# Kernel optimization log

Hardware: AMD Instinct MI355X
Metric: run time of the kernel (lower is better)

The kernel has to match this reference:

```python
import jax, jax.numpy as jnp
import numpy as np

N = 1024      # number of atoms
L = 64        # latent_size
VOCAB = 20    # vocab_size (len(ATOM_CATEGORIES))


def _lin(key, fan_in, fan_out):
    # mimic torch nn.Linear init: U(-1/sqrt(fan_in), 1/sqrt(fan_in))
    kw, kb = jax.random.split(key)
    s = 1.0 / np.sqrt(fan_in)
    W = jax.random.uniform(kw, (fan_in, fan_out), minval=-s, maxval=s, dtype=jnp.float32)
    b = jax.random.uniform(kb, (fan_out,), minval=-s, maxval=s, dtype=jnp.float32)
    return W, b


def setup_inputs() -> dict:
    key = jax.random.key(0)
    ks = jax.random.split(key, 9)
    We1, be1 = _lin(ks[3], 2 * L + 1, L)   # mlp_e layer 1
    We2, be2 = _lin(ks[4], L, L)           # mlp_e layer 2
    Wh1, bh1 = _lin(ks[5], L + 1, L)       # mlp_h layer 1
    Wh2, bh2 = _lin(ks[6], L, L)           # mlp_h layer 2
    Wo, bo = _lin(ks[7], L, 1)             # output_mlp
    return {
        "atom_categories": jax.random.randint(ks[0], (N,), 0, VOCAB),
        "atom_coordinates": jax.random.normal(ks[1], (N, 3), dtype=jnp.float32),
        "learnable_matrix": jax.random.normal(ks[2], (VOCAB, L), dtype=jnp.float32),
        "We1": We1, "be1": be1, "We2": We2, "be2": be2,
        "Wh1": Wh1, "bh1": bh1, "Wh2": Wh2, "bh2": bh2,
        "Wo": Wo, "bo": bo,
    }


def reference(atom_categories, atom_coordinates, learnable_matrix,
              We1, be1, We2, be2, Wh1, bh1, Wh2, bh2, Wo, bo):
    Z = atom_coordinates
    # init_H: learnable_matrix.T @ one_hot(cat) == row gather
    H = learnable_matrix[atom_categories]                       # [N, L]

    # pairwise squared distances ||Z_i - Z_j||^2
    d2 = jnp.sum((Z[:, None, :] - Z[None, :, :]) ** 2, axis=-1)  # [N, N]

    # mlp_e layer 1 on concat(H_i, H_j, d2): split We1 to avoid materializing concat
    W1i, W1j, w1z = We1[:L], We1[L:2 * L], We1[2 * L]            # [L,L],[L,L],[L]
    pre_i = H @ W1i                                              # [N, L]
    pre_j = H @ W1j                                              # [N, L]
    h1 = jnp.tanh(pre_i[:, None, :] + pre_j[None, :, :]
                  + d2[:, :, None] * w1z + be1)                  # [N, N, L]
    W_e = jnp.tanh(h1 @ We2 + be2)                               # [N, N, L]

    # V[i] = sum over j != i of sum_l W_e[i,j,l]
    total = jnp.sum(W_e, axis=(1, 2))                            # [N]
    diag = jnp.einsum('iil->i', W_e)                             # [N]
    V = total - diag                                             # [N]

    # mlp_h on concat(H_i, V_i): split Wh1
    hh = jnp.tanh(H @ Wh1[:L] + V[:, None] * Wh1[L] + bh1)       # [N, L]
    newH = jnp.tanh(hh @ Wh2 + bh2)                              # [N, L]

    Hsum = jnp.sum(newH, axis=0)                                 # [L]
    return (Hsum @ Wo + bo)[0]                                   # scalar
```

## Files before the change

### kernel.cpp

```cpp
#include <hip/hip_runtime.h>
#include <hip/hip_bf16.h>


#define N_ATOMS 1024
#define L_DIM 64
#define TPB 512
#define CSCALE 2.8853900817779268f

typedef _Float16 f16x8 __attribute__((ext_vector_type(8)));
typedef __fp16  fp16x2 __attribute__((ext_vector_type(2)));
typedef float f32x4 __attribute__((ext_vector_type(4)));

__device__ __forceinline__ float tanh_fast(float x) {
    float e = __builtin_amdgcn_exp2f(x * CSCALE);
    float r = __builtin_amdgcn_rcpf(e + 1.0f);
    return fmaf(-2.0f, r, 1.0f);
}

__global__ __launch_bounds__(256) void k_prep(const int* __restrict__ cat,
                                              const float* __restrict__ LM,
                                              const float* __restrict__ We1,
                                              const float* __restrict__ be1,
                                              float* __restrict__ H,
                                              float* __restrict__ preI,
                                              float* __restrict__ P3,
                                              float* __restrict__ out) {
    int t = threadIdx.x;
    int sub = t >> 6, l = t & 63;
    int i = blockIdx.x * 4 + sub;
    if (blockIdx.x == 0 && t == 0) out[0] = 0.f;
    __shared__ float hrow[4][L_DIM];
    float hv = LM[cat[i] * L_DIM + l];
    hrow[sub][l] = hv;
    H[i * L_DIM + l] = hv;
    __syncthreads();
    float s1 = 0.f, s2 = 0.f;
#pragma unroll
    for (int m = 0; m < L_DIM; m++) {
        float h = hrow[sub][m];
        s1 = fmaf(h, We1[m * L_DIM + l], s1);
        s2 = fmaf(h, We1[(L_DIM + m) * L_DIM + l], s2);
    }
    preI[i * L_DIM + l] = s1 * CSCALE;
    int cc = i >> 4;
    int Ll = i & 15;
    int quad = (l >> 3) & 3;
    int L = quad * 16 + Ll;
    int g = ((l >> 5) << 1) | ((l >> 2) & 1);
    int e2 = l & 3;
    P3[cc * 1024 + g * 256 + L * 4 + e2] = (s2 + be1[l]) * CSCALE;
}

__global__ __launch_bounds__(TPB) void k_main(const float* __restrict__ Z,
                                              const float* __restrict__ We1,
                                              const float* __restrict__ We2,
                                              const float* __restrict__ be2,
                                              const float* __restrict__ preI,
                                              const float* __restrict__ P3,
                                              const float* __restrict__ H,
                                              const float* __restrict__ Wh1,
                                              const float* __restrict__ bh1,
                                              const float* __restrict__ Wh2,
                                              const float* __restrict__ bh2,
                                              const float* __restrict__ Wo,
                                              const float* __restrict__ bo,
                                              float* __restrict__ out) {
    int i = blockIdx.x;
    int t = threadIdx.x;
    int lane = t & 63;
    int wave = t >> 6;
    int nlo = lane & 15;
    int quad = lane >> 4;

    __shared__ float d2s[N_ATOMS];
    __shared__ float red[TPB];
    __shared__ float hrow_s[L_DIM];
    __shared__ float hh_s[L_DIM];
    __shared__ float dgt[L_DIM];
    __shared__ f16x8 bLs[8 * 64];

    float zi0 = Z[i * 3], zi1 = Z[i * 3 + 1], zi2 = Z[i * 3 + 2];
    for (int p = t; p < N_ATOMS; p += TPB) {
        float a = zi0 - Z[p * 3], b = zi1 - Z[p * 3 + 1], c = zi2 - Z[p * 3 + 2];
        d2s[p] = a * a + b * b + c * c;
    }

    f32x4 aiR[4], wzR[4];
#pragma unroll
    for (int g = 0; g < 4; g++) {
        int mb = ((g >> 1) << 5) + (quad << 3) + ((g & 1) << 2);
        aiR[g] = *(const f32x4*)(preI + i * L_DIM + mb);
        f32x4 wz = *(const f32x4*)(We1 + 2 * L_DIM * L_DIM + mb);
        wzR[g] = wz * CSCALE;
    }

    f16x8 bH[4][2];
    float biasR[4];
#pragma unroll
    for (int nt = 0; nt < 4; nt++) {
        float psum = 0.f;
#pragma unroll
        for (int kt = 0; kt < 2; kt++) {
            f16x8 hi8, lo8;
#pragma unroll
            for (int e = 0; e < 8; e++) {
                float x = We2[(kt * 32 + quad * 8 + e) * L_DIM + nt * 16 + nlo];
                psum += x;
                float wp = -2.0f * CSCALE * x;
                _Float16 hi = (_Float16)wp;
                hi8[e] = hi;
                lo8[e] = (_Float16)(wp - (float)hi);
            }
            bH[nt][kt] = hi8;
            if (wave == 0) bLs[(kt * 4 + nt) * 64 + lane] = lo8;
        }
        psum += __shfl_xor(psum, 16);
        psum += __shfl_xor(psum, 32);
        biasR[nt] = CSCALE * (be2[nt * 16 + nlo] + psum);
    }

    const float* Pbase = P3 + (wave * 8) * 1024 + lane * 4;
    f32x4 p0 = *(const f32x4*)(Pbase + 0 * 256) + aiR[0];
    f32x4 p1 = *(const f32x4*)(Pbase + 1 * 256) + aiR[1];
    f32x4 p2 = *(const f32x4*)(Pbase + 2 * 256) + aiR[2];
    f32x4 p3 = *(const f32x4*)(Pbase + 3 * 256) + aiR[3];

    __syncthreads();

    f32x4 Vr4 = {0.f, 0.f, 0.f, 0.f};
    for (int k = 0; k < 8; k++) {
        int j0 = (wave * 8 + k) * 16;
        float d2 = d2s[j0 + nlo];
        f32x4 d2v = {d2, d2, d2, d2};

        f32x4 z0 = p0 + d2v * wzR[0];
        f32x4 z1 = p1 + d2v * wzR[1];
        f32x4 z2 = p2 + d2v * wzR[2];
        f32x4 z3 = p3 + d2v * wzR[3];
        f32x4 ex0, ex1, ex2, ex3;
#pragma unroll
        for (int e = 0; e < 4; e++) {
            ex0[e] = __builtin_amdgcn_exp2f(z0[e]);
            ex1[e] = __builtin_amdgcn_exp2f(z1[e]);
            ex2[e] = __builtin_amdgcn_exp2f(z2[e]);
            ex3[e] = __builtin_amdgcn_exp2f(z3[e]);
        }
        ex0 += 1.0f; ex1 += 1.0f; ex2 += 1.0f; ex3 += 1.0f;
        f32x4 r0, r1, r2, r3;
#pragma unroll
        for (int e = 0; e < 4; e++) {
            r0[e] = __builtin_amdgcn_rcpf(ex0[e]);
            r1[e] = __builtin_amdgcn_rcpf(ex1[e]);
            r2[e] = __builtin_amdgcn_rcpf(ex2[e]);
            r3[e] = __builtin_amdgcn_rcpf(ex3[e]);
        }
        union { f16x8 v; fp16x2 h2[4]; } u0, u1;
        u0.h2[0] = __builtin_amdgcn_cvt_pkrtz(r0[0], r0[1]);
        u0.h2[1] = __builtin_amdgcn_cvt_pkrtz(r0[2], r0[3]);
        u0.h2[2] = __builtin_amdgcn_cvt_pkrtz(r1[0], r1[1]);
        u0.h2[3] = __builtin_amdgcn_cvt_pkrtz(r1[2], r1[3]);
        u1.h2[0] = __builtin_amdgcn_cvt_pkrtz(r2[0], r2[1]);
        u1.h2[1] = __builtin_amdgcn_cvt_pkrtz(r2[2], r2[3]);
        u1.h2[2] = __builtin_amdgcn_cvt_pkrtz(r3[0], r3[1]);
        u1.h2[3] = __builtin_amdgcn_cvt_pkrtz(r3[2], r3[3]);
        f16x8 aH0 = u0.v, aH1 = u1.v;

        if (k < 7) {
            const float* nb = Pbase + (k + 1) * 1024;
            p0 = *(const f32x4*)(nb + 0 * 256) + aiR[0];
            p1 = *(const f32x4*)(nb + 1 * 256) + aiR[1];
            p2 = *(const f32x4*)(nb + 2 * 256) + aiR[2];
            p3 = *(const f32x4*)(nb + 3 * 256) + aiR[3];
        }

#pragma unroll
        for (int nt = 0; nt < 4; nt++) {
            f16x8 bl0 = bLs[(0 * 4 + nt) * 64 + lane];
            f16x8 bl1 = bLs[(1 * 4 + nt) * 64 + lane];
            f32x4 acc = {biasR[nt], biasR[nt], biasR[nt], biasR[nt]};
            acc = __builtin_amdgcn_mfma_f32_16x16x32_f16(aH0, bH[nt][0], acc, 0, 0, 0);
            acc = __builtin_amdgcn_mfma_f32_16x16x32_f16(aH0, bl0, acc, 0, 0, 0);
            acc = __builtin_amdgcn_mfma_f32_16x16x32_f16(aH1, bH[nt][1], acc, 0, 0, 0);
            acc = __builtin_amdgcn_mfma_f32_16x16x32_f16(aH1, bl1, acc, 0, 0, 0);
            f32x4 ev;
#pragma unroll
            for (int r4 = 0; r4 < 4; r4++) ev[r4] = __builtin_amdgcn_exp2f(acc[r4]);
            ev += 1.0f;
            f32x4 rv;
#pragma unroll
            for (int r4 = 0; r4 < 4; r4++) rv[r4] = __builtin_amdgcn_rcpf(ev[r4]);
            Vr4 += rv;
        }
    }

    red[t] = Vr4[0] + Vr4[1] + Vr4[2] + Vr4[3];
    __syncthreads();

    float Rall;
    if (t < 64) {
        float r = red[t];
#pragma unroll
        for (int w = 1; w < 8; w++) r += red[t + 64 * w];
#pragma unroll
        for (int o = 32; o > 0; o >>= 1) r += __shfl_xor(r, o);
        Rall = r;
        int cc = i >> 4, Ll = i & 15;
        int q2 = (t >> 3) & 3;
        int g = ((t >> 5) << 1) | ((t >> 2) & 1);
        float z = preI[i * L_DIM + t] + P3[cc * 1024 + g * 256 + (q2 * 16 + Ll) * 4 + (t & 3)];
        float rr = __builtin_amdgcn_rcpf(__builtin_amdgcn_exp2f(z) + 1.0f);
        dgt[t] = fmaf(-2.0f, rr, 1.0f);
        hrow_s[t] = H[i * L_DIM + t];
    }
    __syncthreads();
    if (t < 64) {
        float S = be2[t];
#pragma unroll
        for (int m = 0; m < L_DIM; m++) S = fmaf(dgt[m], We2[m * L_DIM + t], S);
        float rd = __builtin_amdgcn_rcpf(__builtin_amdgcn_exp2f(S * CSCALE) + 1.0f);
#pragma unroll
        for (int o = 32; o > 0; o >>= 1) rd += __shfl_xor(rd, o);
        float V = fmaf(-2.0f, Rall - rd, (float)(1023 * L_DIM));
        float s = 0.f;
#pragma unroll
        for (int m = 0; m < L_DIM; m++) s = fmaf(hrow_s[m], Wh1[m * L_DIM + t], s);
        s = fmaf(V, Wh1[L_DIM * L_DIM + t], s) + bh1[t];
        hh_s[t] = tanh_fast(s);
    }
    __syncthreads();
    if (t < 64) {
        float s2 = 0.f;
#pragma unroll
        for (int m = 0; m < L_DIM; m++) s2 = fmaf(hh_s[m], Wh2[m * L_DIM + t], s2);
        float nh = tanh_fast(s2 + bh2[t]);
        float w = nh * Wo[t];
#pragma unroll
        for (int o = 32; o > 0; o >>= 1) w += __shfl_down(w, o);
        if (t == 0) atomicAdd(out, w + (i == 0 ? bo[0] : 0.f));
    }
}

extern "C" void kernel_launch(void* const* d_in, const int* in_sizes, int n_in,
                              void* d_out, int out_size, void* d_ws, size_t ws_size,
                              hipStream_t stream) {
    const int*   cat = (const int*)  d_in[0];
    const float* Z   = (const float*)d_in[1];
    const float* LM  = (const float*)d_in[2];
    const float* We1 = (const float*)d_in[3];
    const float* be1 = (const float*)d_in[4];
    const float* We2 = (const float*)d_in[5];
    const float* be2 = (const float*)d_in[6];
    const float* Wh1 = (const float*)d_in[7];
    const float* bh1 = (const float*)d_in[8];
    const float* Wh2 = (const float*)d_in[9];
    const float* bh2 = (const float*)d_in[10];
    const float* Wo  = (const float*)d_in[11];
    const float* bo  = (const float*)d_in[12];
    float* out = (float*)d_out;

    float* ws   = (float*)d_ws;
    float* H    = ws;
    float* preI = H    + N_ATOMS * L_DIM;
    float* P3   = preI + N_ATOMS * L_DIM;

    k_prep<<<N_ATOMS / 4, 256, 0, stream>>>(cat, LM, We1, be1, H, preI, P3, out);
    k_main<<<N_ATOMS, TPB, 0, stream>>>(Z, We1, We2, be2, preI, P3, H,
                                        Wh1, bh1, Wh2, bh2, Wo, bo, out);
}
```

Measured before the change: 142.5 us.

## Split main kernel into half-row blocks, precompute weight fragments, move tail to post kernel

The per-atom main kernel now runs as two 256-thread blocks per atom, each covering half of the j range and accumulating partial sums into a global Vpart array with atomics. The fp16 hi/lo split of We2 and the bias terms are computed once in the prep kernel and loaded from global memory instead of being rebuilt by every block. The serial per-atom MLP tail moves into a separate post kernel that handles four atoms per block. This aims at better occupancy and less redundant setup, at the cost of an extra kernel launch and the atomic partial-sum traffic.

```diff
diff --git a/kernel.cpp b/kernel.cpp
--- a/kernel.cpp
+++ b/kernel.cpp
@@ -4,7 +4,6 @@
 
 #define N_ATOMS 1024
 #define L_DIM 64
-#define TPB 512
 #define CSCALE 2.8853900817779268f
 
 typedef _Float16 f16x8 __attribute__((ext_vector_type(8)));
@@ -21,14 +20,21 @@
                                               const float* __restrict__ LM,
                                               const float* __restrict__ We1,
                                               const float* __restrict__ be1,
+                                              const float* __restrict__ We2,
+                                              const float* __restrict__ be2,
                                               float* __restrict__ H,
                                               float* __restrict__ preI,
                                               float* __restrict__ P3,
+                                              float* __restrict__ Vpart,
+                                              f16x8* __restrict__ bHg,
+                                              f16x8* __restrict__ bLg,
+                                              float* __restrict__ biasg,
                                               float* __restrict__ out) {
     int t = threadIdx.x;
     int sub = t >> 6, l = t & 63;
     int i = blockIdx.x * 4 + sub;
     if (blockIdx.x == 0 && t == 0) out[0] = 0.f;
+    if (t < 4) Vpart[blockIdx.x * 4 + t] = 0.f;
     __shared__ float hrow[4][L_DIM];
     float hv = LM[cat[i] * L_DIM + l];
     hrow[sub][l] = hv;
@@ -49,77 +55,83 @@
     int g = ((l >> 5) << 1) | ((l >> 2) & 1);
     int e2 = l & 3;
     P3[cc * 1024 + g * 256 + L * 4 + e2] = (s2 + be1[l]) * CSCALE;
-}
-
-__global__ __launch_bounds__(TPB) void k_main(const float* __restrict__ Z,
-                                              const float* __restrict__ We1,
-                                              const float* __restrict__ We2,
-                                              const float* __restrict__ be2,
-                                              const float* __restrict__ preI,
-                                              const float* __restrict__ P3,
-                                              const float* __restrict__ H,
-                                              const float* __restrict__ Wh1,
-                                              const float* __restrict__ bh1,
-                                              const float* __restrict__ Wh2,
-                                              const float* __restrict__ bh2,
-                                              const float* __restrict__ Wo,
-                                              const float* __restrict__ bo,
-                                              float* __restrict__ out) {
-    int i = blockIdx.x;
-    int t = threadIdx.x;
-    int lane = t & 63;
-    int wave = t >> 6;
-    int nlo = lane & 15;
-    int quad = lane >> 4;
-
-    __shared__ float d2s[N_ATOMS];
-    __shared__ float red[TPB];
-    __shared__ float hrow_s[L_DIM];
-    __shared__ float hh_s[L_DIM];
-    __shared__ float dgt[L_DIM];
-    __shared__ f16x8 bLs[8 * 64];
-
-    float zi0 = Z[i * 3], zi1 = Z[i * 3 + 1], zi2 = Z[i * 3 + 2];
-    for (int p = t; p < N_ATOMS; p += TPB) {
-        float a = zi0 - Z[p * 3], b = zi1 - Z[p * 3 + 1], c = zi2 - Z[p * 3 + 2];
-        d2s[p] = a * a + b * b + c * c;
-    }
-
-    f32x4 aiR[4], wzR[4];
-#pragma unroll
-    for (int g = 0; g < 4; g++) {
-        int mb = ((g >> 1) << 5) + (quad << 3) + ((g & 1) << 2);
-        aiR[g] = *(const f32x4*)(preI + i * L_DIM + mb);
-        f32x4 wz = *(const f32x4*)(We1 + 2 * L_DIM * L_DIM + mb);
-        wzR[g] = wz * CSCALE;
-    }
-
-    f16x8 bH[4][2];
-    float biasR[4];
-#pragma unroll
-    for (int nt = 0; nt < 4; nt++) {
+
+    if (blockIdx.x == 0) {
+        int nt = t >> 6;
+        int lane = t & 63;
+        int q2 = lane >> 4, nl2 = lane & 15;
         float psum = 0.f;
 #pragma unroll
         for (int kt = 0; kt < 2; kt++) {
             f16x8 hi8, lo8;
 #pragma unroll
             for (int e = 0; e < 8; e++) {
-                float x = We2[(kt * 32 + quad * 8 + e) * L_DIM + nt * 16 + nlo];
+                float x = We2[(kt * 32 + q2 * 8 + e) * L_DIM + nt * 16 + nl2];
                 psum += x;
                 float wp = -2.0f * CSCALE * x;
                 _Float16 hi = (_Float16)wp;
                 hi8[e] = hi;
                 lo8[e] = (_Float16)(wp - (float)hi);
             }
-            bH[nt][kt] = hi8;
-            if (wave == 0) bLs[(kt * 4 + nt) * 64 + lane] = lo8;
+            bHg[(kt * 4 + nt) * 64 + lane] = hi8;
+            bLg[(kt * 4 + nt) * 64 + lane] = lo8;
         }
         psum += __shfl_xor(psum, 16);
         psum += __shfl_xor(psum, 32);
-        biasR[nt] = CSCALE * (be2[nt * 16 + nlo] + psum);
-    }
-
-    const float* Pbase = P3 + (wave * 8) * 1024 + lane * 4;
+        biasg[lane * 4 + nt] = CSCALE * (be2[nt * 16 + nl2] + psum);
+    }
+}
+
+__global__ __launch_bounds__(256) void k_main(const float* __restrict__ Z,
+                                              const float* __restrict__ We1,
+                                              const float* __restrict__ preI,
+                                              const float* __restrict__ P3,
+                                              const f16x8* __restrict__ bHg,
+                                              const f16x8* __restrict__ bLg,
+                                              const float* __restrict__ biasg,
+                                              float* __restrict__ Vpart) {
+    int bid = blockIdx.x;
+    int i = bid >> 1, half = bid & 1;
+    int t = threadIdx.x;
+    int lane = t & 63;
+    int wave = t >> 6;
+    int nlo = lane & 15;
+    int quad = lane >> 4;
+
+    __shared__ float d2s[512];
+    __shared__ float red[256];
+    __shared__ f16x8 bLs[8 * 64];
+
+    float zi0 = Z[i * 3], zi1 = Z[i * 3 + 1], zi2 = Z[i * 3 + 2];
+    for (int p = t; p < 512; p += 256) {
+        int j = half * 512 + p;
+        float a = zi0 - Z[j * 3], b = zi1 - Z[j * 3 + 1], c = zi2 - Z[j * 3 + 2];
+        d2s[p] = a * a + b * b + c * c;
+    }
+
+    f32x4 aiR[4], wzR[4];
+#pragma unroll
+    for (int g = 0; g < 4; g++) {
+        int mb = ((g >> 1) << 5) + (quad << 3) + ((g & 1) << 2);
+        aiR[g] = *(const f32x4*)(preI + i * L_DIM + mb);
+        f32x4 wz = *(const f32x4*)(We1 + 2 * L_DIM * L_DIM + mb);
+        wzR[g] = wz * CSCALE;
+    }
+
+    f16x8 bH[4][2];
+#pragma unroll
+    for (int nt = 0; nt < 4; nt++) {
+        bH[nt][0] = bHg[(0 * 4 + nt) * 64 + lane];
+        bH[nt][1] = bHg[(1 * 4 + nt) * 64 + lane];
+    }
+#pragma unroll
+    for (int idx = 0; idx < 2; idx++) {
+        int e = wave + idx * 4;
+        bLs[e * 64 + lane] = bLg[e * 64 + lane];
+    }
+    f32x4 bias4 = *(const f32x4*)(biasg + lane * 4);
+
+    const float* Pbase = P3 + (half * 32 + wave * 8) * 1024 + lane * 4;
     f32x4 p0 = *(const f32x4*)(Pbase + 0 * 256) + aiR[0];
     f32x4 p1 = *(const f32x4*)(Pbase + 1 * 256) + aiR[1];
     f32x4 p2 = *(const f32x4*)(Pbase + 2 * 256) + aiR[2];
@@ -129,8 +141,7 @@
 
     f32x4 Vr4 = {0.f, 0.f, 0.f, 0.f};
     for (int k = 0; k < 8; k++) {
-        int j0 = (wave * 8 + k) * 16;
-        float d2 = d2s[j0 + nlo];
+        float d2 = d2s[(wave * 8 + k) * 16 + nlo];
         f32x4 d2v = {d2, d2, d2, d2};
 
         f32x4 z0 = p0 + d2v * wzR[0];
@@ -177,7 +188,7 @@
         for (int nt = 0; nt < 4; nt++) {
             f16x8 bl0 = bLs[(0 * 4 + nt) * 64 + lane];
             f16x8 bl1 = bLs[(1 * 4 + nt) * 64 + lane];
-            f32x4 acc = {biasR[nt], biasR[nt], biasR[nt], biasR[nt]};
+            f32x4 acc = {bias4[nt], bias4[nt], bias4[nt], bias4[nt]};
             acc = __builtin_amdgcn_mfma_f32_16x16x32_f16(aH0, bH[nt][0], acc, 0, 0, 0);
             acc = __builtin_amdgcn_mfma_f32_16x16x32_f16(aH0, bl0, acc, 0, 0, 0);
             acc = __builtin_amdgcn_mfma_f32_16x16x32_f16(aH1, bH[nt][1], acc, 0, 0, 0);
@@ -195,49 +206,66 @@
 
     red[t] = Vr4[0] + Vr4[1] + Vr4[2] + Vr4[3];
     __syncthreads();
-
-    float Rall;
     if (t < 64) {
-        float r = red[t];
-#pragma unroll
-        for (int w = 1; w < 8; w++) r += red[t + 64 * w];
+        float r = red[t] + red[t + 64] + red[t + 128] + red[t + 192];
 #pragma unroll
         for (int o = 32; o > 0; o >>= 1) r += __shfl_xor(r, o);
-        Rall = r;
-        int cc = i >> 4, Ll = i & 15;
-        int q2 = (t >> 3) & 3;
-        int g = ((t >> 5) << 1) | ((t >> 2) & 1);
-        float z = preI[i * L_DIM + t] + P3[cc * 1024 + g * 256 + (q2 * 16 + Ll) * 4 + (t & 3)];
-        float rr = __builtin_amdgcn_rcpf(__builtin_amdgcn_exp2f(z) + 1.0f);
-        dgt[t] = fmaf(-2.0f, rr, 1.0f);
-        hrow_s[t] = H[i * L_DIM + t];
-    }
-    __syncthreads();
-    if (t < 64) {
-        float S = be2[t];
-#pragma unroll
-        for (int m = 0; m < L_DIM; m++) S = fmaf(dgt[m], We2[m * L_DIM + t], S);
-        float rd = __builtin_amdgcn_rcpf(__builtin_amdgcn_exp2f(S * CSCALE) + 1.0f);
-#pragma unroll
-        for (int o = 32; o > 0; o >>= 1) rd += __shfl_xor(rd, o);
-        float V = fmaf(-2.0f, Rall - rd, (float)(1023 * L_DIM));
-        float s = 0.f;
-#pragma unroll
-        for (int m = 0; m < L_DIM; m++) s = fmaf(hrow_s[m], Wh1[m * L_DIM + t], s);
-        s = fmaf(V, Wh1[L_DIM * L_DIM + t], s) + bh1[t];
-        hh_s[t] = tanh_fast(s);
-    }
-    __syncthreads();
-    if (t < 64) {
-        float s2 = 0.f;
-#pragma unroll
-        for (int m = 0; m < L_DIM; m++) s2 = fmaf(hh_s[m], Wh2[m * L_DIM + t], s2);
-        float nh = tanh_fast(s2 + bh2[t]);
-        float w = nh * Wo[t];
-#pragma unroll
-        for (int o = 32; o > 0; o >>= 1) w += __shfl_down(w, o);
-        if (t == 0) atomicAdd(out, w + (i == 0 ? bo[0] : 0.f));
-    }
+        if (t == 0) atomicAdd(Vpart + i, r);
+    }
+}
+
+__global__ __launch_bounds__(256) void k_post(const float* __restrict__ preI,
+                                              const float* __restrict__ P3,
+                                              const float* __restrict__ H,
+                                              const float* __restrict__ We2,
+                                              const float* __restrict__ be2,
+                                              const float* __restrict__ Wh1,
+                                              const float* __restrict__ bh1,
+                                              const float* __restrict__ Wh2,
+                                              const float* __restrict__ bh2,
+                                              const float* __restrict__ Wo,
+                                              const float* __restrict__ bo,
+                                              const float* __restrict__ Vpart,
+                                              float* __restrict__ out) {
+    int t = threadIdx.x;
+    int sub = t >> 6, lane = t & 63;
+    int i = blockIdx.x * 4 + sub;
+    __shared__ float dgt[4][L_DIM];
+    __shared__ float hrow_s[4][L_DIM];
+    __shared__ float hh_s[4][L_DIM];
+
+    float Rall = Vpart[i];
+    int cc = i >> 4, Ll = i & 15;
+    int q2 = (lane >> 3) & 3;
+    int g = ((lane >> 5) << 1) | ((lane >> 2) & 1);
+    float z = preI[i * L_DIM + lane] + P3[cc * 1024 + g * 256 + (q2 * 16 + Ll) * 4 + (lane & 3)];
+    float rr = __builtin_amdgcn_rcpf(__builtin_amdgcn_exp2f(z) + 1.0f);
+    dgt[sub][lane] = fmaf(-2.0f, rr, 1.0f);
+    hrow_s[sub][lane] = H[i * L_DIM + lane];
+    __syncthreads();
+
+    float S = be2[lane];
+#pragma unroll
+    for (int m = 0; m < L_DIM; m++) S = fmaf(dgt[sub][m], We2[m * L_DIM + lane], S);
+    float rd = __builtin_amdgcn_rcpf(__builtin_amdgcn_exp2f(S * CSCALE) + 1.0f);
+#pragma unroll
+    for (int o = 32; o > 0; o >>= 1) rd += __shfl_xor(rd, o);
+    float V = fmaf(-2.0f, Rall - rd, (float)(1023 * L_DIM));
+    float s = 0.f;
+#pragma unroll
+    for (int m = 0; m < L_DIM; m++) s = fmaf(hrow_s[sub][m], Wh1[m * L_DIM + lane], s);
+    s = fmaf(V, Wh1[L_DIM * L_DIM + lane], s) + bh1[lane];
+    hh_s[sub][lane] = tanh_fast(s);
+    __syncthreads();
+
+    float s2 = 0.f;
+#pragma unroll
+    for (int m = 0; m < L_DIM; m++) s2 = fmaf(hh_s[sub][m], Wh2[m * L_DIM + lane], s2);
+    float nh = tanh_fast(s2 + bh2[lane]);
+    float w = nh * Wo[lane];
+#pragma unroll
+    for (int o = 32; o > 0; o >>= 1) w += __shfl_down(w, o);
+    if (lane == 0) atomicAdd(out, w + (i == 0 ? bo[0] : 0.f));
 }
 
 extern "C" void kernel_launch(void* const* d_in, const int* in_sizes, int n_in,
@@ -258,12 +286,18 @@
     const float* bo  = (const float*)d_in[12];
     float* out = (float*)d_out;
 
-    float* ws   = (float*)d_ws;
-    float* H    = ws;
-    float* preI = H    + N_ATOMS * L_DIM;
-    float* P3   = preI + N_ATOMS * L_DIM;
-
-    k_prep<<<N_ATOMS / 4, 256, 0, stream>>>(cat, LM, We1, be1, H, preI, P3, out);
-    k_main<<<N_ATOMS, TPB, 0, stream>>>(Z, We1, We2, be2, preI, P3, H,
-                                        Wh1, bh1, Wh2, bh2, Wo, bo, out);
-}
+    float* ws    = (float*)d_ws;
+    float* H     = ws;
+    float* preI  = H     + N_ATOMS * L_DIM;
+    float* P3    = preI  + N_ATOMS * L_DIM;
+    float* Vpart = P3    + N_ATOMS * L_DIM;
+    float* biasg = Vpart + N_ATOMS;
+    f16x8* bHg   = (f16x8*)(biasg + 256);
+    f16x8* bLg   = bHg + 8 * 64;
+
+    k_prep<<<N_ATOMS / 4, 256, 0, stream>>>(cat, LM, We1, be1, We2, be2,
+                                            H, preI, P3, Vpart, bHg, bLg, biasg, out);
+    k_main<<<N_ATOMS * 2, 256, 0, stream>>>(Z, We1, preI, P3, bHg, bLg, biasg, Vpart);
+    k_post<<<N_ATOMS / 4, 256, 0, stream>>>(preI, P3, H, We2, be2,
+                                            Wh1, bh1, Wh2, bh2, Wo, bo, Vpart, out);
+}
```

Measured after the change: 137.3 us. 3.6% less time.
